# Kernel optimization log

Hardware: AMD Instinct MI355X
Metric: run time of the kernel (lower is better)

The kernel has to match this reference:

```python
import jax, jax.numpy as jnp
import numpy as np

EMBED_DIM = 1024
HEAD_DIM = 64
B, S = 4, 4096


def setup_inputs() -> dict:
    key = jax.random.key(0)
    ks = jax.random.split(key, 9)
    scale = 1.0 / np.sqrt(EMBED_DIM)
    return {
        "Q": jax.random.normal(ks[0], (B, S, EMBED_DIM), jnp.float32),
        "K": jax.random.normal(ks[1], (B, S, EMBED_DIM), jnp.float32),
        "V": jax.random.normal(ks[2], (B, S, EMBED_DIM), jnp.float32),
        "mask": jnp.ones((1, S, S), jnp.int32),
        "Wq": jax.random.normal(ks[3], (EMBED_DIM, HEAD_DIM), jnp.float32) * scale,
        "bq": jax.random.normal(ks[4], (HEAD_DIM,), jnp.float32) * scale,
        "Wk": jax.random.normal(ks[5], (EMBED_DIM, HEAD_DIM), jnp.float32) * scale,
        "bk": jax.random.normal(ks[6], (HEAD_DIM,), jnp.float32) * scale,
        "Wv": jax.random.normal(ks[7], (EMBED_DIM, HEAD_DIM), jnp.float32) * scale,
        "bv": jax.random.normal(ks[8], (HEAD_DIM,), jnp.float32) * scale,
    }


def reference(Q, K, V, mask, Wq, bq, Wk, bk, Wv, bv):
    # Per-head projections: [B,S,E] @ [E,D] -> [B,S,D]
    q = Q @ Wq + bq
    k = K @ Wk + bk
    v = V @ Wv + bv
    d_k = q.shape[-1]
    # scores: [B,Sq,Sk]
    scores = jnp.einsum("bqd,bkd->bqk", q, k) / jnp.sqrt(jnp.float32(d_k))
    scores = jnp.where(mask == 0, -jnp.inf, scores)
    p_attn = jax.nn.softmax(scores, axis=-1)
    return jnp.einsum("bqk,bkd->bqd", p_attn, v)
```

## Files before the change

kernel.cpp:

```cpp
#include <hip/hip_runtime.h>

#define B_ 4
#define S_ 4096
#define E_ 1024
#define D_ 64

typedef __attribute__((ext_vector_type(8))) short short8;
typedef __attribute__((ext_vector_type(4))) float floatx4;
typedef __attribute__((ext_vector_type(4))) unsigned int uint4v;

__device__ __forceinline__ floatx4 mfma_bf16(short8 a, short8 b, floatx4 c) {
    return __builtin_amdgcn_mfma_f32_16x16x32_bf16(a, b, c, 0, 0, 0);
}

__device__ __forceinline__ short f2bf(float f) {
    unsigned u = __builtin_bit_cast(unsigned, f);
    u = (u + 0x7FFFu + ((u >> 16) & 1u)) >> 16;
    return (short)u;
}

__device__ __forceinline__ unsigned pk2bf(float a, float b) {
    unsigned ua = __builtin_bit_cast(unsigned, a);
    unsigned ub = __builtin_bit_cast(unsigned, b);
    ua = (ua + 0x7FFFu + ((ua >> 16) & 1u)) >> 16;
    ub = (ub + 0x7FFFu + ((ub >> 16) & 1u)) & 0xFFFF0000u;
    return ua | ub;
}

__device__ __forceinline__ void gload_lds16(const void* g, void* l) {
    __builtin_amdgcn_global_load_lds(
        (const __attribute__((address_space(1))) void*)g,
        (__attribute__((address_space(3))) void*)l, 16, 0, 0);
}

__global__ __launch_bounds__(256) void prep_kernel(
    const float* __restrict__ Wq, const float* __restrict__ Wk, const float* __restrict__ Wv,
    short* __restrict__ WT, int* __restrict__ flag)
{
    int tid = blockIdx.x * 256 + threadIdx.x;
    if (tid == 0) *flag = 0;
    int mat = tid >> 16;
    int rem = tid & 65535;
    const float* W = (mat == 0) ? Wq : ((mat == 1) ? Wk : Wv);
    int n = rem >> 10, k = rem & 1023;
    WT[mat * 65536 + n * E_ + k] = f2bf(W[k * D_ + n]);
}

__global__ __launch_bounds__(256, 2) void proj_kernel(
    const float* __restrict__ Qm, const float* __restrict__ Km, const float* __restrict__ Vm,
    const short* __restrict__ WT,
    const float* __restrict__ bq, const float* __restrict__ bk, const float* __restrict__ bv,
    short* __restrict__ qs, short* __restrict__ ks, short* __restrict__ vT,
    const int4* __restrict__ mask4, int* __restrict__ flag)
{
    __shared__ __align__(16) char smem[65536];
    float* of = (float*)(smem + 32768);

    const int mat = blockIdx.y;
    const int bx  = blockIdx.x;
    const int tid = threadIdx.x;
    const int wv = tid >> 6, lane = tid & 63;
    const int quad = lane >> 4, c16 = lane & 15;
    const int rt = wv & 1, kh = wv >> 1;
    const int m0 = bx * 32 + rt * 16;

    const float* X    = (mat == 0) ? Qm : ((mat == 1) ? Km : Vm);
    const float* bias = (mat == 0) ? bq : ((mat == 1) ? bk : bv);
    const char*  Xp   = (const char*)X;

    char* wlds = smem + wv * 16384;

    #define ASTAGE(c_) do {                                              \
        const size_t koff_ = (size_t)kh * 2048 + (size_t)(c_) * 1024;    \
        _Pragma("unroll")                                                \
        for (int i_ = 0; i_ < 16; ++i_) {                                \
            gload_lds16(Xp + (size_t)(m0 + i_) * 4096 + koff_            \
                           + (size_t)((lane ^ (i_ & 7)) << 4),           \
                        wlds + i_ * 1024);                               \
        }                                                                \
    } while (0)

    const short* wk = WT + mat * 65536 + (size_t)c16 * 1024 + quad * 8 + kh * 512;
    #define WLOADM(n_, dst_) do {                                        \
        _Pragma("unroll")                                                \
        for (int f_ = 0; f_ < 4; ++f_)                                   \
            dst_[f_] = *(const short8*)(wk + (n_) * 32 + f_ * 16384);    \
    } while (0)

    floatx4 acc[4];
    #pragma unroll
    for (int f = 0; f < 4; ++f) acc[f] = (floatx4){0.f, 0.f, 0.f, 0.f};
    short8 wA[4], wB[4];

    const char* ardA = wlds + c16 * 1024 + (size_t)(((2 * quad)     ^ (c16 & 7)) << 4);
    const char* ardB = wlds + c16 * 1024 + (size_t)(((2 * quad + 1) ^ (c16 & 7)) << 4);

    #define ASTEP(s_, n_, W_) do {                                       \
        float4 fa_ = *(const float4*)(ardA + (s_) * 128);                \
        float4 fb_ = *(const float4*)(ardB + (s_) * 128);                \
        uint4v uv_;                                                      \
        uv_[0] = pk2bf(fa_.x, fa_.y); uv_[1] = pk2bf(fa_.z, fa_.w);      \
        uv_[2] = pk2bf(fb_.x, fb_.y); uv_[3] = pk2bf(fb_.z, fb_.w);      \
        short8 a_ = __builtin_bit_cast(short8, uv_);                     \
        _Pragma("unroll")                                                \
        for (int f_ = 0; f_ < 4; ++f_)                                   \
            acc[f_] = mfma_bf16(a_, W_[f_], acc[f_]);                    \
        if ((n_) + 2 < 16) WLOADM((n_) + 2, W_);                         \
    } while (0)

    WLOADM(0, wA);
    ASTAGE(0);
    WLOADM(1, wB);
    asm volatile("s_waitcnt vmcnt(0)" ::: "memory");

    ASTEP(0, 0, wA); ASTEP(1, 1, wB); ASTEP(2, 2, wA); ASTEP(3, 3, wB);
    ASTEP(4, 4, wA); ASTEP(5, 5, wB); ASTEP(6, 6, wA); ASTEP(7, 7, wB);

    asm volatile("s_waitcnt lgkmcnt(0)" ::: "memory");
    ASTAGE(1);
    asm volatile("s_waitcnt vmcnt(0)" ::: "memory");

    ASTEP(0,  8, wA); ASTEP(1,  9, wB); ASTEP(2, 10, wA); ASTEP(3, 11, wB);
    ASTEP(4, 12, wA); ASTEP(5, 13, wB); ASTEP(6, 14, wA); ASTEP(7, 15, wB);

    #undef ASTAGE
    #undef WLOADM
    #undef ASTEP

    __syncthreads();
    if (kh == 1) {
        #pragma unroll
        for (int f = 0; f < 4; ++f)
            #pragma unroll
            for (int r = 0; r < 4; ++r)
                of[(rt * 16 + quad * 4 + r) * 68 + f * 16 + c16] = acc[f][r];
    }
    __syncthreads();
    if (kh == 0) {
        const float scale = (mat == 0) ? (0.125f * 1.4426950408889634f) : 1.0f;
        #pragma unroll
        for (int f = 0; f < 4; ++f) {
            float bb = bias[f * 16 + c16];
            if (mat == 2) {
                float v0 = acc[0 + f][0] + of[(rt * 16 + quad * 4 + 0) * 68 + f * 16 + c16] + bb;
                float v1 = acc[f][1] + of[(rt * 16 + quad * 4 + 1) * 68 + f * 16 + c16] + bb;
                float v2 = acc[f][2] + of[(rt * 16 + quad * 4 + 2) * 68 + f * 16 + c16] + bb;
                float v3 = acc[f][3] + of[(rt * 16 + quad * 4 + 3) * 68 + f * 16 + c16] + bb;
                int2 pk = make_int2((int)pk2bf(v0, v1), (int)pk2bf(v2, v3));
                const int lane2 = (rt * 2 + (quad >> 1)) * 16 + c16;
                const int j0 = (quad & 1) * 4;
                *(int2*)(vT + ((size_t)(bx * 4 + f) * 512 + lane2 * 8 + j0)) = pk;
            } else {
                #pragma unroll
                for (int r = 0; r < 4; ++r) {
                    int m = m0 + quad * 4 + r;
                    float v = (acc[f][r] + of[(rt * 16 + quad * 4 + r) * 68 + f * 16 + c16] + bb) * scale;
                    short h = f2bf(v);
                    if (mat == 0) qs[(size_t)m * D_ + f * 16 + c16] = h;
                    else          ks[(size_t)m * D_ + f * 16 + c16] = h;
                }
            }
        }
    }

    {
        int btid = (mat * 512 + bx) * 256 + tid;
        const int stride = 1536 * 256;
        int found = 0;
        for (int i = btid; i < (S_ * S_ / 4); i += stride) {
            int4 v = mask4[i];
            found |= (v.x == 0) | (v.y == 0) | (v.z == 0) | (v.w == 0);
        }
        if (found) atomicOr(flag, 1);
    }
}

__global__ __launch_bounds__(512, 2) void flash_kernel(
    const short* __restrict__ qs, const short* __restrict__ ks,
    const short* __restrict__ vT, const int* __restrict__ mask,
    const int* __restrict__ flag, float* __restrict__ out)
{
    __shared__ __align__(16) char smem[47104];
    short* kst = (short*)smem;
    short* pst = kst + 18432;

    const int bid = blockIdx.x;
    const int b  = (bid & 7) >> 1;
    const int qt = ((bid >> 3) << 1) | (bid & 1);
    const int tid = threadIdx.x;
    const int w = tid >> 6;
    const int qw = w & 1, kwq = w >> 1;
    const int lane = tid & 63;
    const int quad = lane >> 4, c16 = lane & 15;
    const int m0 = qt * 32 + qw * 16;

    const short* qrow = qs + (size_t)(b * S_ + m0 + c16) * D_ + quad * 8;
    short8 aq0 = *(const short8*)(qrow);
    short8 aq1 = *(const short8*)(qrow + 32);

    const short* kbase = ks + (size_t)b * S_ * D_;
    const short* vbase = vT + (size_t)b * 262144 + (size_t)kwq * 65536;

    const int sq   = w >> 1;
    const int srow = (w & 1) * 16 + (lane >> 3);
    const int schunk = lane & 7;
    const short* gstage = kbase + ((size_t)sq * 1024 + srow) * D_ + schunk * 8;
    short* lstage = kst + sq * 2304 + srow * 72 + schunk * 8;

    floatx4 O[4];
    #pragma unroll
    for (int f = 0; f < 4; ++f) O[f] = (floatx4){0.f, 0.f, 0.f, 0.f};
    float lsum = 0.f;

    const int anyz = *flag;
    short* pw = pst + w * 640;
    short8 g0 = *(const short8*)(gstage);
    short8 g1 = *(const short8*)(gstage + 8 * D_);

    for (int kt = 0; kt < 32; ++kt) {
        const int buf = kt & 1;
        *(short8*)(lstage + buf * 9216)           = g0;
        *(short8*)(lstage + buf * 9216 + 8 * 72)  = g1;
        short8 gn0 = g0, gn1 = g1;
        if (kt < 31) {
            gn0 = *(const short8*)(gstage + (size_t)(kt + 1) * 2048);
            gn1 = *(const short8*)(gstage + (size_t)(kt + 1) * 2048 + 8 * D_);
        }
        __syncthreads();

        const int key0 = kt * 32;

        short8 vv[4];
        #pragma unroll
        for (int f = 0; f < 4; ++f)
            vv[f] = *(const short8*)(vbase + (size_t)kt * 2048 + f * 512 + lane * 8);

        const short* kt_lds = kst + buf * 9216 + kwq * 2304;

        floatx4 s[2];
        #pragma unroll
        for (int f = 0; f < 2; ++f) {
            const short* krow = kt_lds + (f * 16 + c16) * 72 + quad * 8;
            short8 ka0 = *(const short8*)(krow);
            short8 ka1 = *(const short8*)(krow + 32);
            floatx4 t = (floatx4){0.f, 0.f, 0.f, 0.f};
            t = mfma_bf16(ka0, aq0, t);
            t = mfma_bf16(ka1, aq1, t);
            s[f] = t;
        }

        if (anyz) {
            #pragma unroll
            for (int f = 0; f < 2; ++f)
                #pragma unroll
                for (int r = 0; r < 4; ++r)
                    if (mask[(size_t)(m0 + c16) * S_ +
                             kwq * 1024 + key0 + f * 16 + quad * 4 + r] == 0)
                        s[f][r] = -__builtin_inff();
        }

        #pragma unroll
        for (int f = 0; f < 2; ++f) {
            float p0 = exp2f(s[f][0]), p1 = exp2f(s[f][1]);
            float p2 = exp2f(s[f][2]), p3 = exp2f(s[f][3]);
            lsum += (p0 + p1) + (p2 + p3);
            int2 pk = make_int2((int)pk2bf(p0, p1), (int)pk2bf(p2, p3));
            *(int2*)(pw + c16 * 40 + f * 16 + quad * 4) = pk;
        }

        short8 pa = *(const short8*)(pw + c16 * 40 + quad * 8);

        #pragma unroll
        for (int f = 0; f < 4; ++f) O[f] = mfma_bf16(pa, vv[f], O[f]);
        g0 = gn0; g1 = gn1;
    }

    lsum += __shfl_xor(lsum, 16);
    lsum += __shfl_xor(lsum, 32);

    __syncthreads();
    float* of = (float*)smem;
    float* lw = (float*)(smem + 34816);
    #pragma unroll
    for (int f = 0; f < 4; ++f)
        #pragma unroll
        for (int r = 0; r < 4; ++r)
            of[(kwq * 32 + qw * 16 + quad * 4 + r) * 68 + f * 16 + c16] = O[f][r];
    if (quad == 0) lw[kwq * 32 + qw * 16 + c16] = lsum;
    __syncthreads();

    {
        const int q = tid >> 4;
        const int col0 = (tid & 15) * 4;
        const float inv = 1.0f / (lw[q] + lw[32 + q] + lw[64 + q] + lw[96 + q]);
        float4 o = *(const float4*)&of[q * 68 + col0];
        #pragma unroll
        for (int k = 1; k < 4; ++k) {
            float4 t = *(const float4*)&of[(k * 32 + q) * 68 + col0];
            o.x += t.x; o.y += t.y; o.z += t.z; o.w += t.w;
        }
        o.x *= inv; o.y *= inv; o.z *= inv; o.w *= inv;
        *(float4*)(out + ((size_t)(b * S_ + qt * 32 + q)) * 64 + col0) = o;
    }
}

extern "C" void kernel_launch(void* const* d_in, const int* in_sizes, int n_in,
                              void* d_out, int out_size, void* d_ws, size_t ws_size,
                              hipStream_t stream)
{
    const float* Q   = (const float*)d_in[0];
    const float* K   = (const float*)d_in[1];
    const float* V   = (const float*)d_in[2];
    const int*  mask = (const int*) d_in[3];
    const float* Wq  = (const float*)d_in[4];
    const float* bq  = (const float*)d_in[5];
    const float* Wk  = (const float*)d_in[6];
    const float* bk  = (const float*)d_in[7];
    const float* Wv  = (const float*)d_in[8];
    const float* bv  = (const float*)d_in[9];
    float* out = (float*)d_out;

    short* qs = (short*)d_ws;
    short* ks = qs + (size_t)B_ * S_ * D_;
    short* vT = ks + (size_t)B_ * S_ * D_;
    short* WT = vT + (size_t)B_ * S_ * D_;
    int* flag = (int*)(WT + 3 * D_ * E_);

    prep_kernel<<<768, 256, 0, stream>>>(Wq, Wk, Wv, WT, flag);
    proj_kernel<<<dim3(512, 3), 256, 0, stream>>>(Q, K, V, WT, bq, bk, bv,
                                                  qs, ks, vT, (const int4*)mask, flag);
    flash_kernel<<<512, 512, 0, stream>>>(qs, ks, vT, mask, flag, out);
}
```

Measured before the change: 307.8 us.

## Halve projection LDS staging to raise occupancy and use nontemporal streaming loads

The projection kernel's per-wave LDS staging buffer is halved by loading the activation K-slice in four stages of 512 bytes instead of two of 1024. This cuts shared memory per block from 64KB to 32KB, and launch bounds now request 4 blocks per CU instead of 2. The global-to-LDS loads and the mask scan now use nontemporal cache hints so streamed data does not pollute the cache. The trade-off is more wait points between load and compute stages, which could expose latency.

```diff
diff --git a/kernel.cpp b/kernel.cpp
--- a/kernel.cpp
+++ b/kernel.cpp
@@ -8,6 +8,7 @@
 typedef __attribute__((ext_vector_type(8))) short short8;
 typedef __attribute__((ext_vector_type(4))) float floatx4;
 typedef __attribute__((ext_vector_type(4))) unsigned int uint4v;
+typedef __attribute__((ext_vector_type(4))) int intx4;
 
 __device__ __forceinline__ floatx4 mfma_bf16(short8 a, short8 b, floatx4 c) {
     return __builtin_amdgcn_mfma_f32_16x16x32_bf16(a, b, c, 0, 0, 0);
@@ -27,10 +28,10 @@
     return ua | ub;
 }
 
-__device__ __forceinline__ void gload_lds16(const void* g, void* l) {
+__device__ __forceinline__ void gload_lds16_nt(const void* g, void* l) {
     __builtin_amdgcn_global_load_lds(
         (const __attribute__((address_space(1))) void*)g,
-        (__attribute__((address_space(3))) void*)l, 16, 0, 0);
+        (__attribute__((address_space(3))) void*)l, 16, 0, 2);
 }
 
 __global__ __launch_bounds__(256) void prep_kernel(
@@ -46,15 +47,15 @@
     WT[mat * 65536 + n * E_ + k] = f2bf(W[k * D_ + n]);
 }
 
-__global__ __launch_bounds__(256, 2) void proj_kernel(
+__global__ __launch_bounds__(256, 4) void proj_kernel(
     const float* __restrict__ Qm, const float* __restrict__ Km, const float* __restrict__ Vm,
     const short* __restrict__ WT,
     const float* __restrict__ bq, const float* __restrict__ bk, const float* __restrict__ bv,
     short* __restrict__ qs, short* __restrict__ ks, short* __restrict__ vT,
-    const int4* __restrict__ mask4, int* __restrict__ flag)
+    const int* __restrict__ maskp, int* __restrict__ flag)
 {
-    __shared__ __align__(16) char smem[65536];
-    float* of = (float*)(smem + 32768);
+    __shared__ __align__(16) char smem[32768];
+    float* of = (float*)(smem + 16384);
 
     const int mat = blockIdx.y;
     const int bx  = blockIdx.x;
@@ -68,23 +69,26 @@
     const float* bias = (mat == 0) ? bq : ((mat == 1) ? bk : bv);
     const char*  Xp   = (const char*)X;
 
-    char* wlds = smem + wv * 16384;
-
-    #define ASTAGE(c_) do {                                              \
-        const size_t koff_ = (size_t)kh * 2048 + (size_t)(c_) * 1024;    \
-        _Pragma("unroll")                                                \
-        for (int i_ = 0; i_ < 16; ++i_) {                                \
-            gload_lds16(Xp + (size_t)(m0 + i_) * 4096 + koff_            \
-                           + (size_t)((lane ^ (i_ & 7)) << 4),           \
-                        wlds + i_ * 1024);                               \
-        }                                                                \
+    char* wlds = smem + wv * 8192;
+
+    const int srow2 = lane >> 5;
+    const int sg    = lane & 31;
+    #define ASTAGE(c_) do {                                                   \
+        const size_t koff_ = (size_t)kh * 2048 + (size_t)(c_) * 512;          \
+        _Pragma("unroll")                                                     \
+        for (int j_ = 0; j_ < 8; ++j_) {                                      \
+            const int row_ = 2 * j_ + srow2;                                  \
+            gload_lds16_nt(Xp + (size_t)(m0 + row_) * 4096 + koff_            \
+                              + (size_t)((sg ^ (row_ & 7)) << 4),             \
+                           wlds + j_ * 1024);                                 \
+        }                                                                     \
     } while (0)
 
     const short* wk = WT + mat * 65536 + (size_t)c16 * 1024 + quad * 8 + kh * 512;
-    #define WLOADM(n_, dst_) do {                                        \
-        _Pragma("unroll")                                                \
-        for (int f_ = 0; f_ < 4; ++f_)                                   \
-            dst_[f_] = *(const short8*)(wk + (n_) * 32 + f_ * 16384);    \
+    #define WLOADM(n_, dst_) do {                                             \
+        _Pragma("unroll")                                                     \
+        for (int f_ = 0; f_ < 4; ++f_)                                        \
+            dst_[f_] = *(const short8*)(wk + (n_) * 32 + f_ * 16384);         \
     } while (0)
 
     floatx4 acc[4];
@@ -92,36 +96,42 @@
     for (int f = 0; f < 4; ++f) acc[f] = (floatx4){0.f, 0.f, 0.f, 0.f};
     short8 wA[4], wB[4];
 
-    const char* ardA = wlds + c16 * 1024 + (size_t)(((2 * quad)     ^ (c16 & 7)) << 4);
-    const char* ardB = wlds + c16 * 1024 + (size_t)(((2 * quad + 1) ^ (c16 & 7)) << 4);
-
-    #define ASTEP(s_, n_, W_) do {                                       \
-        float4 fa_ = *(const float4*)(ardA + (s_) * 128);                \
-        float4 fb_ = *(const float4*)(ardB + (s_) * 128);                \
-        uint4v uv_;                                                      \
-        uv_[0] = pk2bf(fa_.x, fa_.y); uv_[1] = pk2bf(fa_.z, fa_.w);      \
-        uv_[2] = pk2bf(fb_.x, fb_.y); uv_[3] = pk2bf(fb_.z, fb_.w);      \
-        short8 a_ = __builtin_bit_cast(short8, uv_);                     \
-        _Pragma("unroll")                                                \
-        for (int f_ = 0; f_ < 4; ++f_)                                   \
-            acc[f_] = mfma_bf16(a_, W_[f_], acc[f_]);                    \
-        if ((n_) + 2 < 16) WLOADM((n_) + 2, W_);                         \
+    const char* ardA = wlds + c16 * 512 + (size_t)(((2 * quad)     ^ (c16 & 7)) << 4);
+    const char* ardB = wlds + c16 * 512 + (size_t)(((2 * quad + 1) ^ (c16 & 7)) << 4);
+
+    #define ASTEP(s_, n_, W_) do {                                            \
+        float4 fa_ = *(const float4*)(ardA + (s_) * 128);                     \
+        float4 fb_ = *(const float4*)(ardB + (s_) * 128);                     \
+        uint4v uv_;                                                           \
+        uv_[0] = pk2bf(fa_.x, fa_.y); uv_[1] = pk2bf(fa_.z, fa_.w);           \
+        uv_[2] = pk2bf(fb_.x, fb_.y); uv_[3] = pk2bf(fb_.z, fb_.w);           \
+        short8 a_ = __builtin_bit_cast(short8, uv_);                          \
+        _Pragma("unroll")                                                     \
+        for (int f_ = 0; f_ < 4; ++f_)                                        \
+            acc[f_] = mfma_bf16(a_, W_[f_], acc[f_]);                         \
+        if ((n_) + 2 < 16) WLOADM((n_) + 2, W_);                              \
     } while (0)
 
-    WLOADM(0, wA);
     ASTAGE(0);
-    WLOADM(1, wB);
+    WLOADM(0, wA); WLOADM(1, wB);
     asm volatile("s_waitcnt vmcnt(0)" ::: "memory");
 
     ASTEP(0, 0, wA); ASTEP(1, 1, wB); ASTEP(2, 2, wA); ASTEP(3, 3, wB);
-    ASTEP(4, 4, wA); ASTEP(5, 5, wB); ASTEP(6, 6, wA); ASTEP(7, 7, wB);
-
     asm volatile("s_waitcnt lgkmcnt(0)" ::: "memory");
     ASTAGE(1);
     asm volatile("s_waitcnt vmcnt(0)" ::: "memory");
 
-    ASTEP(0,  8, wA); ASTEP(1,  9, wB); ASTEP(2, 10, wA); ASTEP(3, 11, wB);
-    ASTEP(4, 12, wA); ASTEP(5, 13, wB); ASTEP(6, 14, wA); ASTEP(7, 15, wB);
+    ASTEP(0, 4, wA); ASTEP(1, 5, wB); ASTEP(2, 6, wA); ASTEP(3, 7, wB);
+    asm volatile("s_waitcnt lgkmcnt(0)" ::: "memory");
+    ASTAGE(2);
+    asm volatile("s_waitcnt vmcnt(0)" ::: "memory");
+
+    ASTEP(0, 8, wA); ASTEP(1, 9, wB); ASTEP(2, 10, wA); ASTEP(3, 11, wB);
+    asm volatile("s_waitcnt lgkmcnt(0)" ::: "memory");
+    ASTAGE(3);
+    asm volatile("s_waitcnt vmcnt(0)" ::: "memory");
+
+    ASTEP(0, 12, wA); ASTEP(1, 13, wB); ASTEP(2, 14, wA); ASTEP(3, 15, wB);
 
     #undef ASTAGE
     #undef WLOADM
@@ -142,7 +152,7 @@
         for (int f = 0; f < 4; ++f) {
             float bb = bias[f * 16 + c16];
             if (mat == 2) {
-                float v0 = acc[0 + f][0] + of[(rt * 16 + quad * 4 + 0) * 68 + f * 16 + c16] + bb;
+                float v0 = acc[f][0] + of[(rt * 16 + quad * 4 + 0) * 68 + f * 16 + c16] + bb;
                 float v1 = acc[f][1] + of[(rt * 16 + quad * 4 + 1) * 68 + f * 16 + c16] + bb;
                 float v2 = acc[f][2] + of[(rt * 16 + quad * 4 + 2) * 68 + f * 16 + c16] + bb;
                 float v3 = acc[f][3] + of[(rt * 16 + quad * 4 + 3) * 68 + f * 16 + c16] + bb;
@@ -167,8 +177,9 @@
         int btid = (mat * 512 + bx) * 256 + tid;
         const int stride = 1536 * 256;
         int found = 0;
+        const intx4* m4 = (const intx4*)maskp;
         for (int i = btid; i < (S_ * S_ / 4); i += stride) {
-            int4 v = mask4[i];
+            intx4 v = __builtin_nontemporal_load(m4 + i);
             found |= (v.x == 0) | (v.y == 0) | (v.z == 0) | (v.w == 0);
         }
         if (found) atomicOr(flag, 1);
@@ -328,6 +339,6 @@
 
     prep_kernel<<<768, 256, 0, stream>>>(Wq, Wk, Wv, WT, flag);
     proj_kernel<<<dim3(512, 3), 256, 0, stream>>>(Q, K, V, WT, bq, bk, bv,
-                                                  qs, ks, vT, (const int4*)mask, flag);
+                                                  qs, ks, vT, mask, flag);
     flash_kernel<<<512, 512, 0, stream>>>(qs, ks, vT, mask, flag, out);
 }
```

Result: faster. 297.4 us (-3.4%).
